# Kernel tuning notes

Measured on AMD Instinct MI355X. Metric: run time of the kernel, lower is better.

The kernel has to match this reference:

```python
import jax, jax.numpy as jnp
import numpy as np

B, L, H, E = 4, 2048, 8, 64
WINDOW = 8
DILATION = 1


def setup_inputs() -> dict:
    key = jax.random.key(0)
    kq, kk, kv, ka = jax.random.split(key, 4)
    queries = jax.random.normal(kq, (B, L, H, E), dtype=jnp.float32)
    keys = jax.random.normal(kk, (B, L, H, E), dtype=jnp.float32)
    values = jax.random.normal(kv, (B, L, H, E), dtype=jnp.float32)
    alpha = jax.random.uniform(ka, (1,), dtype=jnp.float32)
    return {"queries": queries, "keys": keys, "values": values, "alpha": alpha}


def _full_attention(q, k, v, scale):
    # q,k,v: [B, L, H, E]
    scores = jnp.einsum('blhe,bshe->bhls', q, k) * scale  # [B,H,L,L]
    A = jax.nn.softmax(scores, axis=-1)
    return jnp.einsum('bhls,bshd->blhd', A, v)


def _local_attention(q, k, v, scale):
    # efficient gather-based local window attention, non-causal
    Lk = k.shape[1]
    offsets = jnp.arange(-WINDOW, WINDOW + 1) * DILATION
    idx = jnp.clip(jnp.arange(Lk)[:, None] + offsets[None, :], 0, Lk - 1)
    K_win = k[:, idx]
    V_win = v[:, idx]
    scores = jnp.einsum('blhe,blwhe->blhw', q, K_win) * scale
    A = jax.nn.softmax(scores, axis=-1)
    return jnp.einsum('blhw,blwhe->blhe', A, V_win)


def reference(queries, keys, values, alpha):
    scale = 1.0 / np.sqrt(queries.shape[-1]).astype(np.float32)
    out_full = _full_attention(queries, keys, values, scale)
    out_local = _local_attention(queries, keys, values, scale)
    w = jax.nn.sigmoid(alpha[0])
    # only_target_first=True: positions 1..L-1 take out_full, position 0 is gated
    out = out_full.at[:, 0].set(w * out_full[:, 0] + (1.0 - w) * out_local[:, 0])
    return out
```

## Files before the change

kernel.cpp:

```cpp
#include <hip/hip_runtime.h>

typedef unsigned short u16;
typedef unsigned int   u32;
typedef __attribute__((ext_vector_type(8))) short short8;
typedef __attribute__((ext_vector_type(4))) float f32x4;

#define MFMA16(a, b, c) __builtin_amdgcn_mfma_f32_16x16x32_bf16(a, b, c, 0, 0, 0)

constexpr int Lv = 2048, Hv = 8, Ev = 64, HE = Hv * Ev;
constexpr float QSCALE = 0.18033688011112042f;

__device__ __forceinline__ float bf2f(u16 u) {
    u32 x = ((u32)u) << 16;
    return __builtin_bit_cast(float, x);
}
__device__ __forceinline__ u16 f2bf(float f) {
    u32 x = __builtin_bit_cast(u32, f);
    u32 r = ((x >> 16) & 1u) + 0x7fffu;
    return (u16)((x + r) >> 16);
}
__device__ __forceinline__ u32 pkbf(float a, float b) {
#if __has_builtin(__builtin_amdgcn_cvt_pk_bf16_f32)
    typedef __attribute__((ext_vector_type(2))) __bf16 bf16x2;
    bf16x2 v = __builtin_amdgcn_cvt_pk_bf16_f32(a, b);
    return __builtin_bit_cast(u32, v);
#else
    return (u32)f2bf(a) | ((u32)f2bf(b) << 16);
#endif
}
__device__ __forceinline__ float fexp2(float x) {
#if __has_builtin(__builtin_amdgcn_exp2f)
    return __builtin_amdgcn_exp2f(x);
#else
    return exp2f(x);
#endif
}

__device__ __forceinline__ int detect_isbf16(const u32* q32, int lane) {
    u32 w0 = q32[2 * lane];
    u32 w1 = q32[2 * lane + 1];
    u16 uu[4] = { (u16)(w0 & 0xffff), (u16)(w0 >> 16),
                  (u16)(w1 & 0xffff), (u16)(w1 >> 16) };
    int p = 0, z = 0;
#pragma unroll
    for (int j = 0; j < 4; ++j) {
        u16 mgn = (u16)(uu[j] & 0x7fff);
        int ex  = mgn >> 7;
        bool zero = (mgn == 0);
        bool pl   = zero || (ex >= 115 && ex <= 132);
        p += pl ? 1 : 0;
        if ((j & 1) == 0) z += zero ? 1 : 0;
    }
    int acc = p | (z << 16);
#pragma unroll
    for (int o = 1; o < 64; o <<= 1) acc += __shfl_xor(acc, o);
    int ps = acc & 0xffff, zs = acc >> 16;
    if (zs >= 100) return 0;
    return (ps >= 240) ? 1 : 0;
}

__device__ __forceinline__ short8 cvt8s(const float* p, float s) {
    float4 a = *(const float4*)p, b4 = *(const float4*)(p + 4);
    u32 r[4] = { pkbf(a.x * s, a.y * s), pkbf(a.z * s, a.w * s),
                 pkbf(b4.x * s, b4.y * s), pkbf(b4.z * s, b4.w * s) };
    return *(short8*)r;
}

template <int ISBF>
__device__ __forceinline__ void attn_impl(
    const void* __restrict__ qv, const void* __restrict__ kv,
    const void* __restrict__ vv, const void* __restrict__ alphav,
    void* __restrict__ outv, u16* Klds, u16* Vt, u16* PldsAll)
{
    const int tid  = threadIdx.x;
    const int w    = tid >> 6;
    const int lane = tid & 63;
    const int quad = lane >> 4;
    const int m    = lane & 15;

    const int fid = blockIdx.x;
    const int bh  = (fid & 7) * 4 + ((fid >> 3) & 3);
    const int rb  = fid >> 5;
    const int b   = bh >> 3, h = bh & 7;
    const int row0 = rb * 128;

    const size_t bhoff = (size_t)b * Lv * HE + h * Ev;
    const u16*   q16 = (const u16*)qv + bhoff;
    const u16*   k16 = (const u16*)kv + bhoff;
    const u16*   v16 = (const u16*)vv + bhoff;
    const float* q32 = (const float*)qv + bhoff;
    const float* k32 = (const float*)kv + bhoff;
    const float* v32 = (const float*)vv + bhoff;

    short8 qf[2];
    {
        size_t ro = (size_t)(row0 + w * 16 + m) * HE + quad * 8;
        if (ISBF) {
            short8 t0 = *(const short8*)(q16 + ro);
            short8 t1 = *(const short8*)(q16 + ro + 32);
#pragma unroll
            for (int j = 0; j < 8; ++j) {
                qf[0][j] = (short)f2bf(bf2f((u16)t0[j]) * QSCALE);
                qf[1][j] = (short)f2bf(bf2f((u16)t1[j]) * QSCALE);
            }
        } else {
            qf[0] = cvt8s(q32 + ro, QSCALE);
            qf[1] = cvt8s(q32 + ro + 32, QSCALE);
        }
    }

    short8 ones8;
#pragma unroll
    for (int j = 0; j < 8; ++j) ones8[j] = (short)0x3F80;

    f32x4 O[4];
    f32x4 Ssum = f32x4{0.f, 0.f, 0.f, 0.f};
#pragma unroll
    for (int et = 0; et < 4; ++et) O[et] = f32x4{0.f, 0.f, 0.f, 0.f};

    const int kkey = tid >> 3, ksl = tid & 7;
    const int koff = kkey * HE + (ksl ^ (kkey & 7)) * 8;
    const int eq = tid & 15, pp = tid >> 4;
    const int kcv = pp >> 2, pq = pp & 3;

    u16* Pw = PldsAll + w * 1024;

    float4 kfa, kfb, vfa, vfb;
    uint4  kru; uint2 vru0, vru1;

#define LOAD_TILE(KT)                                                          \
    do {                                                                       \
        if (ISBF) {                                                            \
            kru  = *(const uint4*)(k16 + (size_t)(KT) * 64 * HE + koff);       \
            const u16* vp_ = v16 + (size_t)((KT) * 64 + 2 * pp) * HE + eq * 4; \
            vru0 = *(const uint2*)vp_;                                         \
            vru1 = *(const uint2*)(vp_ + HE);                                  \
        } else {                                                               \
            const float* kp_ = k32 + (size_t)(KT) * 64 * HE + koff;            \
            kfa = *(const float4*)kp_;                                         \
            kfb = *(const float4*)(kp_ + 4);                                   \
            const float* vp_ = v32 + (size_t)((KT) * 64 + 2 * pp) * HE + eq * 4;\
            vfa = *(const float4*)vp_;                                         \
            vfb = *(const float4*)(vp_ + HE);                                  \
        }                                                                      \
    } while (0)

#define STORE_TILE(KB, VB)                                                     \
    do {                                                                       \
        if (ISBF) {                                                            \
            *(uint4*)&(KB)[tid * 8] = kru;                                     \
            const u16* a0_ = (const u16*)&vru0;                                \
            const u16* a1_ = (const u16*)&vru1;                                \
            _Pragma("unroll")                                                  \
            for (int j = 0; j < 4; ++j) {                                      \
                int e_  = eq * 4 + j;                                          \
                int sl_ = kcv ^ ((e_ + (e_ >> 3)) & 7);                        \
                u32 val_ = (u32)a0_[j] | ((u32)a1_[j] << 16);                  \
                *(u32*)&(VB)[e_ * 64 + sl_ * 8 + pq * 2] = val_;               \
            }                                                                  \
        } else {                                                               \
            u32 kk_[4] = { pkbf(kfa.x, kfa.y), pkbf(kfa.z, kfa.w),             \
                           pkbf(kfb.x, kfb.y), pkbf(kfb.z, kfb.w) };           \
            *(uint4*)&(KB)[tid * 8] = *(uint4*)kk_;                            \
            float t0_[4] = {vfa.x, vfa.y, vfa.z, vfa.w};                       \
            float t1_[4] = {vfb.x, vfb.y, vfb.z, vfb.w};                       \
            _Pragma("unroll")                                                  \
            for (int j = 0; j < 4; ++j) {                                      \
                int e_  = eq * 4 + j;                                          \
                int sl_ = kcv ^ ((e_ + (e_ >> 3)) & 7);                        \
                *(u32*)&(VB)[e_ * 64 + sl_ * 8 + pq * 2] = pkbf(t0_[j], t1_[j]);\
            }                                                                  \
        }                                                                      \
    } while (0)

    LOAD_TILE(0);
    STORE_TILE(Klds, Vt);
    __syncthreads();

    for (int kt = 0; kt < 32; ++kt) {
        u16* Kb = Klds + (kt & 1) * 4096;
        u16* Vb = Vt   + (kt & 1) * 4096;
        u16* Kn = Klds + ((kt & 1) ^ 1) * 4096;
        u16* Vn = Vt   + ((kt & 1) ^ 1) * 4096;

        if (kt < 31) LOAD_TILE(kt + 1);

        f32x4 St[4];
#pragma unroll
        for (int nt = 0; nt < 4; ++nt) St[nt] = f32x4{0.f, 0.f, 0.f, 0.f};
#pragma unroll
        for (int c = 0; c < 2; ++c) {
#pragma unroll
            for (int nt = 0; nt < 4; ++nt) {
                int krow = nt * 16 + m;
                int sl   = (4 * c + quad) ^ (m & 7);
                short8 kf = *(const short8*)&Kb[krow * 64 + sl * 8];
                St[nt] = MFMA16(kf, qf[c], St[nt]);
            }
        }

#pragma unroll
        for (int nt = 0; nt < 4; ++nt) {
            u32 u0 = pkbf(fexp2(St[nt][0]), fexp2(St[nt][1]));
            u32 u1 = pkbf(fexp2(St[nt][2]), fexp2(St[nt][3]));
            int G   = 2 * nt + (quad >> 1);
            int off = m * 64 + ((G ^ (m & 7)) * 8) + (quad & 1) * 4;
            uint2 val; val.x = u0; val.y = u1;
            *(uint2*)&Pw[off] = val;
        }

#pragma unroll
        for (int c = 0; c < 2; ++c) {
            int Gp = (4 * c + quad) ^ (m & 7);
            short8 pf = *(const short8*)&Pw[m * 64 + Gp * 8];
            Ssum = MFMA16(pf, ones8, Ssum);
#pragma unroll
            for (int et = 0; et < 4; ++et) {
                int e  = et * 16 + m;
                int sl = (4 * c + quad) ^ ((e + (e >> 3)) & 7);
                short8 vf = *(const short8*)&Vb[e * 64 + sl * 8];
                O[et] = MFMA16(pf, vf, O[et]);
            }
        }

        if (kt < 31) {
            STORE_TILE(Kn, Vn);
            __syncthreads();
        }
    }
#undef LOAD_TILE
#undef STORE_TILE

    float locv[4] = {0.f, 0.f, 0.f, 0.f};
    float wgt = 0.f;
    const bool isrow0 = (rb == 0) && (w == 0) && (quad == 0);
    if (rb == 0 && w == 0) {
        const int e = lane;
        const size_t base = bhoff + e;
#define LDIN(p, i) (ISBF ? bf2f(((const u16*)(p))[i]) : ((const float*)(p))[i])
        float qe = LDIN(qv, base);
        float s[9];
#pragma unroll
        for (int j = 0; j < 9; ++j) {
            float prod = qe * LDIN(kv, base + (size_t)j * HE);
#pragma unroll
            for (int o = 1; o < 64; o <<= 1) prod += __shfl_xor(prod, o);
            s[j] = prod * 0.125f;
        }
        float mx = s[0];
#pragma unroll
        for (int j = 1; j < 9; ++j) mx = fmaxf(mx, s[j]);
        float we[9];
#pragma unroll
        for (int j = 0; j < 9; ++j) we[j] = expf(s[j] - mx);
        float denom = 9.f * we[0];
        float acc   = 9.f * we[0] * LDIN(vv, base);
#pragma unroll
        for (int j = 1; j < 9; ++j) {
            denom += we[j];
            acc   += we[j] * LDIN(vv, base + (size_t)j * HE);
        }
        float loc = acc / denom;

        float a;
        if (ISBF) {
            a = bf2f(((const u16*)alphav)[0]);
            if (!(a >= 0.0f && a <= 1.0f)) {
                float af = ((const float*)alphav)[0];
                if (af >= 0.0f && af <= 1.0f) a = af;
            }
        } else {
            a = ((const float*)alphav)[0];
            if (!(a >= 0.0f && a <= 1.0f)) {
                float ab = bf2f(((const u16*)alphav)[0]);
                if (ab >= 0.0f && ab <= 1.0f) a = ab;
            }
        }
        wgt = 1.f / (1.f + expf(-a));
#pragma unroll
        for (int et = 0; et < 4; ++et) locv[et] = __shfl(loc, et * 16 + m);
#undef LDIN
    }

#pragma unroll
    for (int r = 0; r < 4; ++r) {
        float inv = 1.0f / Ssum[r];
        int row = row0 + w * 16 + quad * 4 + r;
        size_t oo = (size_t)(b * Lv + row) * HE + h * Ev + m;
        bool blend = isrow0 && (r == 0);
#pragma unroll
        for (int et = 0; et < 4; ++et) {
            float res = O[et][r] * inv;
            if (blend) res = wgt * res + (1.f - wgt) * locv[et];
            if (ISBF) ((u16*)outv)[oo + et * 16] = f2bf(res);
            else      ((float*)outv)[oo + et * 16] = res;
        }
    }
}

__global__ __launch_bounds__(512, 4) void attn_kernel(
    const void* __restrict__ qv, const void* __restrict__ kv,
    const void* __restrict__ vv, const void* __restrict__ alphav,
    void* __restrict__ outv)
{
    __shared__ u16 Klds[2 * 64 * 64];
    __shared__ u16 Vt[2 * 64 * 64];
    __shared__ u16 Plds[8 * 16 * 64];

    const int isbf = detect_isbf16((const u32*)qv, threadIdx.x & 63);
    if (isbf) attn_impl<1>(qv, kv, vv, alphav, outv, Klds, Vt, Plds);
    else      attn_impl<0>(qv, kv, vv, alphav, outv, Klds, Vt, Plds);
}

extern "C" void kernel_launch(void* const* d_in, const int* in_sizes, int n_in,
                              void* d_out, int out_size, void* d_ws, size_t ws_size,
                              hipStream_t stream) {
    hipLaunchKernelGGL(attn_kernel, dim3(512), dim3(512), 0, stream,
                       d_in[0], d_in[1], d_in[2], d_in[3], d_out);
}
```

Baseline: 144.7 us.

## Switch attention to 32x32 MFMA with register-resident P via permlane swap

Replaces the 16x16x32 bf16 MFMA tiles with 32x32x16 tiles, so each wave handles 32 query rows and blocks drop from 512 to 256 threads. The exponentiated score tile is repacked in registers with permlane32 swaps and fed straight into the PV MFMA, removing the LDS round trip for P. The ones-vector MFMA row sum is replaced by a scalar accumulation with a cross-half shuffle. This raises register pressure and halves threads per block, which may reduce occupancy and latency hiding.

```diff
diff --git a/kernel.cpp b/kernel.cpp
--- a/kernel.cpp
+++ b/kernel.cpp
@@ -3,9 +3,9 @@
 typedef unsigned short u16;
 typedef unsigned int   u32;
 typedef __attribute__((ext_vector_type(8))) short short8;
-typedef __attribute__((ext_vector_type(4))) float f32x4;
-
-#define MFMA16(a, b, c) __builtin_amdgcn_mfma_f32_16x16x32_bf16(a, b, c, 0, 0, 0)
+typedef __attribute__((ext_vector_type(16))) float f32x16;
+
+#define MFMA32(a, b, c) __builtin_amdgcn_mfma_f32_32x32x16_bf16(a, b, c, 0, 0, 0)
 
 constexpr int Lv = 2048, Hv = 8, Ev = 64, HE = Hv * Ev;
 constexpr float QSCALE = 0.18033688011112042f;
@@ -66,17 +66,39 @@
     return *(short8*)r;
 }
 
+__device__ __forceinline__ f32x16 zv16() {
+    f32x16 z;
+#pragma unroll
+    for (int r = 0; r < 16; ++r) z[r] = 0.f;
+    return z;
+}
+
+__device__ __forceinline__ void plswap(u32& a, u32& b) {
+#if __has_builtin(__builtin_amdgcn_permlane32_swap)
+    auto r = __builtin_amdgcn_permlane32_swap(a, b, false, false);
+    a = r[0]; b = r[1];
+#else
+    int lane = (int)(threadIdx.x & 63);
+    u32 ax = (u32)__shfl_xor((int)a, 32);
+    u32 bx = (u32)__shfl_xor((int)b, 32);
+    bool hi = lane >= 32;
+    u32 na = hi ? bx : a;
+    u32 nb = hi ? b  : ax;
+    a = na; b = nb;
+#endif
+}
+
 template <int ISBF>
 __device__ __forceinline__ void attn_impl(
     const void* __restrict__ qv, const void* __restrict__ kv,
     const void* __restrict__ vv, const void* __restrict__ alphav,
-    void* __restrict__ outv, u16* Klds, u16* Vt, u16* PldsAll)
+    void* __restrict__ outv, u16* Klds, u16* Vt)
 {
     const int tid  = threadIdx.x;
     const int w    = tid >> 6;
     const int lane = tid & 63;
-    const int quad = lane >> 4;
-    const int m    = lane & 15;
+    const int l31  = lane & 31;
+    const int hi   = lane >> 5;
 
     const int fid = blockIdx.x;
     const int bh  = (fid & 7) * 4 + ((fid >> 3) & 3);
@@ -92,85 +114,84 @@
     const float* k32 = (const float*)kv + bhoff;
     const float* v32 = (const float*)vv + bhoff;
 
-    short8 qf[2];
+    short8 qf[4];
     {
-        size_t ro = (size_t)(row0 + w * 16 + m) * HE + quad * 8;
+        size_t ro = (size_t)(row0 + w * 32 + l31) * HE + hi * 8;
         if (ISBF) {
-            short8 t0 = *(const short8*)(q16 + ro);
-            short8 t1 = *(const short8*)(q16 + ro + 32);
-#pragma unroll
-            for (int j = 0; j < 8; ++j) {
-                qf[0][j] = (short)f2bf(bf2f((u16)t0[j]) * QSCALE);
-                qf[1][j] = (short)f2bf(bf2f((u16)t1[j]) * QSCALE);
+#pragma unroll
+            for (int c = 0; c < 4; ++c) {
+                short8 t = *(const short8*)(q16 + ro + 16 * c);
+#pragma unroll
+                for (int j = 0; j < 8; ++j)
+                    qf[c][j] = (short)f2bf(bf2f((u16)t[j]) * QSCALE);
             }
         } else {
-            qf[0] = cvt8s(q32 + ro, QSCALE);
-            qf[1] = cvt8s(q32 + ro + 32, QSCALE);
-        }
-    }
-
-    short8 ones8;
-#pragma unroll
-    for (int j = 0; j < 8; ++j) ones8[j] = (short)0x3F80;
-
-    f32x4 O[4];
-    f32x4 Ssum = f32x4{0.f, 0.f, 0.f, 0.f};
-#pragma unroll
-    for (int et = 0; et < 4; ++et) O[et] = f32x4{0.f, 0.f, 0.f, 0.f};
+#pragma unroll
+            for (int c = 0; c < 4; ++c) qf[c] = cvt8s(q32 + ro + 16 * c, QSCALE);
+        }
+    }
+
+    f32x16 O[2];
+    O[0] = zv16(); O[1] = zv16();
+    float psum = 0.f;
 
     const int kkey = tid >> 3, ksl = tid & 7;
     const int koff = kkey * HE + (ksl ^ (kkey & 7)) * 8;
-    const int eq = tid & 15, pp = tid >> 4;
-    const int kcv = pp >> 2, pq = pp & 3;
-
-    u16* Pw = PldsAll + w * 1024;
-
-    float4 kfa, kfb, vfa, vfb;
-    uint4  kru; uint2 vru0, vru1;
-
-#define LOAD_TILE(KT)                                                          \
-    do {                                                                       \
-        if (ISBF) {                                                            \
-            kru  = *(const uint4*)(k16 + (size_t)(KT) * 64 * HE + koff);       \
-            const u16* vp_ = v16 + (size_t)((KT) * 64 + 2 * pp) * HE + eq * 4; \
-            vru0 = *(const uint2*)vp_;                                         \
-            vru1 = *(const uint2*)(vp_ + HE);                                  \
-        } else {                                                               \
-            const float* kp_ = k32 + (size_t)(KT) * 64 * HE + koff;            \
-            kfa = *(const float4*)kp_;                                         \
-            kfb = *(const float4*)(kp_ + 4);                                   \
-            const float* vp_ = v32 + (size_t)((KT) * 64 + 2 * pp) * HE + eq * 4;\
-            vfa = *(const float4*)vp_;                                         \
-            vfb = *(const float4*)(vp_ + HE);                                  \
-        }                                                                      \
+    const int eq = tid & 15, pp0 = tid >> 4;
+    const int kcv0 = pp0 >> 2, pq = pp0 & 3;
+
+    float4 kfa[2], kfb[2], vfa[2], vfb[2];
+    uint4  kru[2]; uint2 vru0[2], vru1[2];
+
+#define LOAD_TILE(KT)                                                           \
+    do {                                                                        \
+        _Pragma("unroll")                                                       \
+        for (int i = 0; i < 2; ++i) {                                           \
+            if (ISBF) {                                                         \
+                kru[i] = *(const uint4*)(k16 + (size_t)(KT) * 64 * HE + koff + i * 32 * HE); \
+                const u16* vp_ = v16 + (size_t)((KT) * 64 + 2 * (pp0 + 16 * i)) * HE + eq * 4; \
+                vru0[i] = *(const uint2*)vp_;                                   \
+                vru1[i] = *(const uint2*)(vp_ + HE);                            \
+            } else {                                                            \
+                const float* kp_ = k32 + (size_t)(KT) * 64 * HE + koff + i * 32 * HE; \
+                kfa[i] = *(const float4*)kp_;                                   \
+                kfb[i] = *(const float4*)(kp_ + 4);                             \
+                const float* vp_ = v32 + (size_t)((KT) * 64 + 2 * (pp0 + 16 * i)) * HE + eq * 4; \
+                vfa[i] = *(const float4*)vp_;                                   \
+                vfb[i] = *(const float4*)(vp_ + HE);                            \
+            }                                                                   \
+        }                                                                       \
     } while (0)
 
-#define STORE_TILE(KB, VB)                                                     \
-    do {                                                                       \
-        if (ISBF) {                                                            \
-            *(uint4*)&(KB)[tid * 8] = kru;                                     \
-            const u16* a0_ = (const u16*)&vru0;                                \
-            const u16* a1_ = (const u16*)&vru1;                                \
-            _Pragma("unroll")                                                  \
-            for (int j = 0; j < 4; ++j) {                                      \
-                int e_  = eq * 4 + j;                                          \
-                int sl_ = kcv ^ ((e_ + (e_ >> 3)) & 7);                        \
-                u32 val_ = (u32)a0_[j] | ((u32)a1_[j] << 16);                  \
-                *(u32*)&(VB)[e_ * 64 + sl_ * 8 + pq * 2] = val_;               \
-            }                                                                  \
-        } else {                                                               \
-            u32 kk_[4] = { pkbf(kfa.x, kfa.y), pkbf(kfa.z, kfa.w),             \
-                           pkbf(kfb.x, kfb.y), pkbf(kfb.z, kfb.w) };           \
-            *(uint4*)&(KB)[tid * 8] = *(uint4*)kk_;                            \
-            float t0_[4] = {vfa.x, vfa.y, vfa.z, vfa.w};                       \
-            float t1_[4] = {vfb.x, vfb.y, vfb.z, vfb.w};                       \
-            _Pragma("unroll")                                                  \
-            for (int j = 0; j < 4; ++j) {                                      \
-                int e_  = eq * 4 + j;                                          \
-                int sl_ = kcv ^ ((e_ + (e_ >> 3)) & 7);                        \
-                *(u32*)&(VB)[e_ * 64 + sl_ * 8 + pq * 2] = pkbf(t0_[j], t1_[j]);\
-            }                                                                  \
-        }                                                                      \
+#define STORE_TILE(KB, VB)                                                      \
+    do {                                                                        \
+        _Pragma("unroll")                                                       \
+        for (int i = 0; i < 2; ++i) {                                           \
+            if (ISBF) {                                                         \
+                *(uint4*)&(KB)[(tid + 256 * i) * 8] = kru[i];                   \
+                const u16* a0_ = (const u16*)&vru0[i];                          \
+                const u16* a1_ = (const u16*)&vru1[i];                          \
+                _Pragma("unroll")                                               \
+                for (int j = 0; j < 4; ++j) {                                   \
+                    int e_  = eq * 4 + j;                                       \
+                    int sl_ = (kcv0 + 4 * i) ^ ((e_ + (e_ >> 3)) & 7);          \
+                    u32 val_ = (u32)a0_[j] | ((u32)a1_[j] << 16);               \
+                    *(u32*)&(VB)[e_ * 64 + sl_ * 8 + pq * 2] = val_;            \
+                }                                                               \
+            } else {                                                            \
+                u32 kk_[4] = { pkbf(kfa[i].x, kfa[i].y), pkbf(kfa[i].z, kfa[i].w), \
+                               pkbf(kfb[i].x, kfb[i].y), pkbf(kfb[i].z, kfb[i].w) }; \
+                *(uint4*)&(KB)[(tid + 256 * i) * 8] = *(uint4*)kk_;             \
+                float t0_[4] = {vfa[i].x, vfa[i].y, vfa[i].z, vfa[i].w};        \
+                float t1_[4] = {vfb[i].x, vfb[i].y, vfb[i].z, vfb[i].w};        \
+                _Pragma("unroll")                                               \
+                for (int j = 0; j < 4; ++j) {                                   \
+                    int e_  = eq * 4 + j;                                       \
+                    int sl_ = (kcv0 + 4 * i) ^ ((e_ + (e_ >> 3)) & 7);          \
+                    *(u32*)&(VB)[e_ * 64 + sl_ * 8 + pq * 2] = pkbf(t0_[j], t1_[j]); \
+                }                                                               \
+            }                                                                   \
+        }                                                                       \
     } while (0)
 
     LOAD_TILE(0);
@@ -185,41 +206,45 @@
 
         if (kt < 31) LOAD_TILE(kt + 1);
 
-        f32x4 St[4];
-#pragma unroll
-        for (int nt = 0; nt < 4; ++nt) St[nt] = f32x4{0.f, 0.f, 0.f, 0.f};
-#pragma unroll
-        for (int c = 0; c < 2; ++c) {
-#pragma unroll
-            for (int nt = 0; nt < 4; ++nt) {
-                int krow = nt * 16 + m;
-                int sl   = (4 * c + quad) ^ (m & 7);
+        f32x16 St[2];
+        St[0] = zv16(); St[1] = zv16();
+#pragma unroll
+        for (int c = 0; c < 4; ++c) {
+#pragma unroll
+            for (int s = 0; s < 2; ++s) {
+                int krow = s * 32 + l31;
+                int sl   = (2 * c + hi) ^ (krow & 7);
                 short8 kf = *(const short8*)&Kb[krow * 64 + sl * 8];
-                St[nt] = MFMA16(kf, qf[c], St[nt]);
-            }
-        }
-
-#pragma unroll
-        for (int nt = 0; nt < 4; ++nt) {
-            u32 u0 = pkbf(fexp2(St[nt][0]), fexp2(St[nt][1]));
-            u32 u1 = pkbf(fexp2(St[nt][2]), fexp2(St[nt][3]));
-            int G   = 2 * nt + (quad >> 1);
-            int off = m * 64 + ((G ^ (m & 7)) * 8) + (quad & 1) * 4;
-            uint2 val; val.x = u0; val.y = u1;
-            *(uint2*)&Pw[off] = val;
-        }
-
-#pragma unroll
-        for (int c = 0; c < 2; ++c) {
-            int Gp = (4 * c + quad) ^ (m & 7);
-            short8 pf = *(const short8*)&Pw[m * 64 + Gp * 8];
-            Ssum = MFMA16(pf, ones8, Ssum);
-#pragma unroll
-            for (int et = 0; et < 4; ++et) {
-                int e  = et * 16 + m;
-                int sl = (4 * c + quad) ^ ((e + (e >> 3)) & 7);
-                short8 vf = *(const short8*)&Vb[e * 64 + sl * 8];
-                O[et] = MFMA16(pf, vf, O[et]);
+                St[s] = MFMA32(kf, qf[c], St[s]);
+            }
+        }
+
+#pragma unroll
+        for (int s = 0; s < 2; ++s) {
+            float pe[16];
+#pragma unroll
+            for (int r = 0; r < 16; ++r) pe[r] = fexp2(St[s][r]);
+#pragma unroll
+            for (int r = 0; r < 16; ++r) psum += pe[r];
+            u32 c8[8];
+#pragma unroll
+            for (int q = 0; q < 8; ++q) c8[q] = pkbf(pe[2 * q], pe[2 * q + 1]);
+#pragma unroll
+            for (int t = 0; t < 2; ++t) {
+                u32 a0 = c8[4 * t + 0], a1 = c8[4 * t + 1];
+                u32 a2 = c8[4 * t + 2], a3 = c8[4 * t + 3];
+                plswap(a0, a2);
+                plswap(a1, a3);
+                u32 pw_[4] = { a0, a1, a2, a3 };
+                short8 pa = *(short8*)pw_;
+                int ks = 2 * s + t;
+#pragma unroll
+                for (int et = 0; et < 2; ++et) {
+                    int e  = et * 32 + l31;
+                    int sl = (2 * ks + hi) ^ ((e + (e >> 3)) & 7);
+                    short8 vf = *(const short8*)&Vb[e * 64 + sl * 8];
+                    O[et] = MFMA32(pa, vf, O[et]);
+                }
             }
         }
 
@@ -231,10 +256,10 @@
 #undef LOAD_TILE
 #undef STORE_TILE
 
-    float locv[4] = {0.f, 0.f, 0.f, 0.f};
+    float locv[2] = {0.f, 0.f};
     float wgt = 0.f;
-    const bool isrow0 = (rb == 0) && (w == 0) && (quad == 0);
-    if (rb == 0 && w == 0) {
+    const bool w0blk = (rb == 0) && (w == 0);
+    if (w0blk) {
         const int e = lane;
         const size_t base = bhoff + e;
 #define LDIN(p, i) (ISBF ? bf2f(((const u16*)(p))[i]) : ((const float*)(p))[i])
@@ -278,43 +303,50 @@
         }
         wgt = 1.f / (1.f + expf(-a));
 #pragma unroll
-        for (int et = 0; et < 4; ++et) locv[et] = __shfl(loc, et * 16 + m);
+        for (int et = 0; et < 2; ++et) locv[et] = __shfl(loc, et * 32 + l31);
 #undef LDIN
     }
 
-#pragma unroll
-    for (int r = 0; r < 4; ++r) {
-        float inv = 1.0f / Ssum[r];
-        int row = row0 + w * 16 + quad * 4 + r;
-        size_t oo = (size_t)(b * Lv + row) * HE + h * Ev + m;
-        bool blend = isrow0 && (r == 0);
-#pragma unroll
-        for (int et = 0; et < 4; ++et) {
-            float res = O[et][r] * inv;
-            if (blend) res = wgt * res + (1.f - wgt) * locv[et];
-            if (ISBF) ((u16*)outv)[oo + et * 16] = f2bf(res);
-            else      ((float*)outv)[oo + et * 16] = res;
-        }
-    }
-}
-
-__global__ __launch_bounds__(512, 4) void attn_kernel(
+    float pst  = psum + __shfl_xor(psum, 32);
+    float invv = 1.0f / pst;
+
+#pragma unroll
+    for (int rg = 0; rg < 4; ++rg) {
+#pragma unroll
+        for (int rr = 0; rr < 4; ++rr) {
+            const int reg = rg * 4 + rr;
+            const int rl  = rr + 8 * rg + 4 * hi;
+            float inv = __shfl(invv, rl);
+            int row = row0 + w * 32 + rl;
+            size_t oo = (size_t)(b * Lv + row) * HE + h * Ev + l31;
+            bool blend = w0blk && (rl == 0);
+#pragma unroll
+            for (int et = 0; et < 2; ++et) {
+                float res = O[et][reg] * inv;
+                if (blend) res = wgt * res + (1.f - wgt) * locv[et];
+                if (ISBF) ((u16*)outv)[oo + et * 32] = f2bf(res);
+                else      ((float*)outv)[oo + et * 32] = res;
+            }
+        }
+    }
+}
+
+__global__ __launch_bounds__(256, 2) void attn_kernel(
     const void* __restrict__ qv, const void* __restrict__ kv,
     const void* __restrict__ vv, const void* __restrict__ alphav,
     void* __restrict__ outv)
 {
     __shared__ u16 Klds[2 * 64 * 64];
     __shared__ u16 Vt[2 * 64 * 64];
-    __shared__ u16 Plds[8 * 16 * 64];
 
     const int isbf = detect_isbf16((const u32*)qv, threadIdx.x & 63);
-    if (isbf) attn_impl<1>(qv, kv, vv, alphav, outv, Klds, Vt, Plds);
-    else      attn_impl<0>(qv, kv, vv, alphav, outv, Klds, Vt, Plds);
+    if (isbf) attn_impl<1>(qv, kv, vv, alphav, outv, Klds, Vt);
+    else      attn_impl<0>(qv, kv, vv, alphav, outv, Klds, Vt);
 }
 
 extern "C" void kernel_launch(void* const* d_in, const int* in_sizes, int n_in,
                               void* d_out, int out_size, void* d_ws, size_t ws_size,
                               hipStream_t stream) {
-    hipLaunchKernelGGL(attn_kernel, dim3(512), dim3(512), 0, stream,
+    hipLaunchKernelGGL(attn_kernel, dim3(512), dim3(256), 0, stream,
                        d_in[0], d_in[1], d_in[2], d_in[3], d_out);
 }
```

Result: slower. 153.7 us (+6.2%).
